# Performance work log

Hardware: AMD Instinct MI355X
Metric: run time of the kernel (lower is better)

Reference implementation:

```python
import jax, jax.numpy as jnp
import numpy as np

NUM_CLASSES = 10
SOFT_CENTER_RADIUS = 3.0
TOPK = 13
IOU_WEIGHT = 3.0
EPS = 1e-07
INF = 100000000.0


def setup_inputs() -> dict:
    key = jax.random.key(0)
    ks = jax.random.split(key, 8)
    B, N, G, C = 8, 16384, 64, NUM_CLASSES
    # priors: [N,4] = (cx, cy, stride_x, stride_y)
    centers = jax.random.uniform(ks[0], (N, 2), minval=0.0, maxval=640.0)
    strides = jnp.full((N, 2), 16.0, dtype=jnp.float32)
    priors = jnp.concatenate([centers, strides], axis=-1)
    # 2D gt boxes (x1,y1,x2,y2) inside a 640px image
    xy = jax.random.uniform(ks[1], (B, G, 2), minval=0.0, maxval=520.0)
    wh = jax.random.uniform(ks[2], (B, G, 2), minval=20.0, maxval=120.0)
    gt_bboxes = jnp.concatenate([xy, xy + wh], axis=-1)
    gt_center = xy + 0.5 * wh
    # 3D boxes: only columns [0,2] (x,z) are used by the dist iou branch
    gt_bboxes_3d = jax.random.normal(ks[3], (B, G, 7)) * 2.0
    pred_bboxes = jax.random.normal(ks[4], (B, N, 7)) * 2.0
    pred_scores = jax.random.normal(ks[5], (B, N, C))
    gt_labels = jax.random.randint(ks[6], (B, G, 1), 0, C, dtype=jnp.int32)
    pad_bbox_flag = jnp.ones((B, G, 1), dtype=jnp.float32)
    return dict(pred_bboxes=pred_bboxes, pred_scores=pred_scores, priors=priors,
                gt_labels=gt_labels, gt_bboxes=gt_bboxes, gt_center=gt_center,
                gt_bboxes_3d=gt_bboxes_3d, pad_bbox_flag=pad_bbox_flag)


def reference(pred_bboxes, pred_scores, priors, gt_labels, gt_bboxes, gt_center,
              gt_bboxes_3d, pad_bbox_flag):
    B, N, _ = pred_bboxes.shape
    G = gt_bboxes.shape[1]

    pc = priors[:, :2]                                   # [N,2]
    # find_inside_points: prior center strictly inside 2D gt box -> [B,N,G]
    cx, cy = pc[None, :, None, 0], pc[None, :, None, 1]
    inside = ((cx > gt_bboxes[:, None, :, 0]) & (cy > gt_bboxes[:, None, :, 1]) &
              (cx < gt_bboxes[:, None, :, 2]) & (cy < gt_bboxes[:, None, :, 3]))
    is_in_gts = inside.astype(jnp.float32) * pad_bbox_flag[:, None, :, 0]  # [B,N,G]
    mask = is_in_gts > 0

    # soft center prior
    strides = priors[None, :, None, 2:]                  # [1,N,1,2]
    diff = (pc[None, :, None, :] - gt_center[:, None, :, :]) / strides
    distance = jnp.linalg.norm(diff, axis=-1) * is_in_gts
    soft_center_prior = 10.0 ** (distance - SOFT_CENTER_RADIUS)

    # dist-type pairwise iou on (x,z) plane
    xz = jnp.array([0, 2])
    pxz = pred_bboxes[:, :, xz]                          # [B,N,2]
    gxz = gt_bboxes_3d[:, :, xz]                         # [B,G,2]
    d = jnp.linalg.norm(pxz[:, :, None, :] - gxz[:, None, :, :], axis=-1)
    pairwise_ious = jnp.clip(1.0 - d / 4.0, 0.0, 1.0)    # [B,N,G]

    iou_cost = -jnp.log(pairwise_ious + EPS) * IOU_WEIGHT

    labels = gt_labels[..., 0]                           # [B,G]
    idx = jnp.broadcast_to(labels[:, None, :], (B, N, G))
    pscores = jnp.take_along_axis(pred_scores, idx, axis=2)  # [B,N,G] logits
    scale = pairwise_ious - jax.nn.sigmoid(pscores)
    # stable BCE-with-logits(pscores, target=pairwise_ious)
    bce = jnp.maximum(pscores, 0.0) - pscores * pairwise_ious + jnp.log1p(jnp.exp(-jnp.abs(pscores)))
    cls_cost = bce * scale ** 2

    cost = jnp.where(mask, cls_cost + iou_cost + soft_center_prior, INF)

    # ---- dynamic k matching ----
    k = min(TOPK, N)
    topk_ious = jax.lax.top_k(jnp.swapaxes(pairwise_ious, 1, 2), k)[0]  # [B,G,k]
    dynamic_ks = jnp.clip(topk_ious.sum(-1).astype(jnp.int32), 1, None)  # [B,G]
    sorted_cost = jnp.sort(cost, axis=1)
    cost_k = jnp.take_along_axis(sorted_cost, dynamic_ks[:, None, :], axis=1)
    cost_k_1 = jnp.take_along_axis(sorted_cost, (dynamic_ks - 1)[:, None, :], axis=1)
    thr = 0.5 * (cost_k + cost_k_1) * is_in_gts          # [B,N,G]
    matching = cost <= thr                               # bool [B,N,G]
    masked_cost = jnp.where(matching, cost, INF)
    multi = matching.sum(-1) > 1                         # prior matched to >1 gt
    argmin_gt = jnp.argmin(masked_cost, axis=2)
    onehot = jax.nn.one_hot(argmin_gt, G, dtype=jnp.bool_)
    matching = jnp.where(multi[..., None], onehot, matching)

    # ---- assemble outputs (dense, jit-friendly version of nonzero indices) ----
    max_index = jnp.argmin(cost, axis=2)                 # [B,N]
    assign_metrics = jnp.take_along_axis(pairwise_ious, max_index[..., None], axis=2)[..., 0]
    matched = matching.any(-1)                           # [B,N]
    gt_idx = jnp.argmax(matching, axis=-1)               # [B,N]
    matched_iou = jnp.take_along_axis(pairwise_ious, gt_idx[..., None], axis=2)[..., 0]
    assign_metrics = jnp.where(matched, matched_iou, assign_metrics)

    assigned_labels = jnp.take_along_axis(labels, max_index, axis=1)  # [B,N]
    assigned_labels = jnp.where(assign_metrics < 1e-07, NUM_CLASSES, assigned_labels)
    assigned_labels = jnp.where(matched, jnp.take_along_axis(labels, gt_idx, axis=1), assigned_labels)

    assigned_labels_weights = jnp.ones((B, N), dtype=jnp.float32)
    return assigned_labels, assigned_labels_weights, assign_metrics, matching
```

## Files before the change

### kernel.cpp

```cpp
#include <hip/hip_runtime.h>
#include <hip/hip_bf16.h>
#include <stdint.h>

#define NCLS 10
#define B_ 8
#define N_ 16384
#define G_ 64
#define INF_ 1.0e8f

typedef unsigned long long u64;
typedef unsigned int u32;

__device__ __forceinline__ u32 ordf(float f) {
    u32 b = __float_as_uint(f);
    return (b & 0x80000000u) ? ~b : (b | 0x80000000u);
}
__device__ __forceinline__ float unordf(u32 u) {
    u32 b = (u & 0x80000000u) ? (u ^ 0x80000000u) : ~u;
    return __uint_as_float(b);
}

__device__ __forceinline__ float iou_pair(float px, float pz, float g3x, float g3z) {
#pragma clang fp contract(off)
    float ddx = px - g3x;
    float ddz = pz - g3z;
    float d = sqrtf(ddx * ddx + ddz * ddz);
    float iou = 1.0f - d / 4.0f;
    return fminf(fmaxf(iou, 0.0f), 1.0f);
}

__device__ __forceinline__ float cost_pair(float cx, float cy, float sx, float sy,
                                           float ps, float gcx, float gcy,
                                           float pad, float iou) {
#pragma clang fp contract(off)
    float dx = (cx - gcx) / sx;
    float dy = (cy - gcy) / sy;
    float dist = sqrtf(dx * dx + dy * dy) * pad;
    float soft = exp10f(dist - 3.0f);
    float iou_cost = -logf(iou + 1e-7f) * 3.0f;
    float e = expf(-fabsf(ps));
    float sig = (ps >= 0.0f) ? (1.0f / (1.0f + e)) : (e / (1.0f + e));
    float scale = iou - sig;
    float bce = fmaxf(ps, 0.0f) - ps * iou + log1pf(e);
    float cls = bce * (scale * scale);
    return cls + iou_cost + soft;
}

__device__ __forceinline__ u32 wave_max_u32(u32 k) {
#pragma unroll
    for (int off = 32; off >= 1; off >>= 1) {
        u32 o = __shfl_xor(k, off, 64);
        k = (o > k) ? o : k;
    }
    return k;
}
__device__ __forceinline__ u32 wave_min_u32(u32 k) {
#pragma unroll
    for (int off = 32; off >= 1; off >>= 1) {
        u32 o = __shfl_xor(k, off, 64);
        k = (o < k) ? o : k;
    }
    return k;
}

__global__ __launch_bounds__(256) void kP(
    const float* __restrict__ priors,
    const float* __restrict__ gt_bboxes,
    const float* __restrict__ pad_flag,
    const float* __restrict__ pred_bboxes,
    u64* __restrict__ mask64,
    u64* __restrict__ bitmapT,
    float2* __restrict__ pxz)
{
    int tid = threadIdx.x;
    int lane = tid & 63;
    if (blockIdx.x < 512) {
        int q = blockIdx.x;
        int b = q >> 6;
        int n = ((q & 63) << 8) | tid;
        u32 wword = ((q & 63) << 2) | (u32)(tid >> 6);
        float4 pr = ((const float4*)priors)[n];
        float cx = pr.x, cy = pr.y;
        u64 m = 0;
        for (int g = 0; g < G_; ++g) {
            int gi = b * G_ + g;
            float4 gbb = ((const float4*)gt_bboxes)[gi];
            float padv = pad_flag[gi];
            bool isin = (cx > gbb.x) && (cy > gbb.y) && (cx < gbb.z) && (cy < gbb.w)
                        && (padv > 0.0f);
            m |= ((u64)isin) << g;
            u64 bal = __ballot(isin);
            if (lane == 0) bitmapT[(((size_t)gi) << 8) | wword] = bal;
        }
        mask64[(size_t)b * N_ + n] = m;
    } else {
        int base = (int)(blockIdx.x - 512) * 2048 + tid;
#pragma unroll
        for (int i = 0; i < 8; ++i) {
            int idx = base + i * 256;
            float2 v;
            v.x = pred_bboxes[(size_t)idx * 7 + 0];
            v.y = pred_bboxes[(size_t)idx * 7 + 2];
            pxz[idx] = v;
        }
    }
}

#define CSWAPD(a, b) { float _h = fmaxf(a, b), _l = fminf(a, b); a = _h; b = _l; }

__global__ __launch_bounds__(256) void k1b(
    const float2* __restrict__ pxz,
    const float* __restrict__ gt_b3d,
    float* __restrict__ iou13)
{
    int wid = ((int)blockIdx.x << 2) | (threadIdx.x >> 6);
    int lane = threadIdx.x & 63;
    int b = wid >> 11;
    int g = (wid >> 5) & 63;
    int chunk = wid & 31;
    int gi = b * G_ + g;
    float g3x = gt_b3d[gi * 7 + 0];
    float g3z = gt_b3d[gi * 7 + 2];
    const float2* pp = pxz + (size_t)b * N_ + (size_t)(chunk * 512 + lane);

    float2 e0 = pp[0],   e1 = pp[64],  e2 = pp[128], e3 = pp[192];
    float2 e4 = pp[256], e5 = pp[320], e6 = pp[384], e7 = pp[448];
    float s0 = iou_pair(e0.x, e0.y, g3x, g3z);
    float s1 = iou_pair(e1.x, e1.y, g3x, g3z);
    float s2 = iou_pair(e2.x, e2.y, g3x, g3z);
    float s3 = iou_pair(e3.x, e3.y, g3x, g3z);
    float s4 = iou_pair(e4.x, e4.y, g3x, g3z);
    float s5 = iou_pair(e5.x, e5.y, g3x, g3z);
    float s6 = iou_pair(e6.x, e6.y, g3x, g3z);
    float s7 = iou_pair(e7.x, e7.y, g3x, g3z);

    CSWAPD(s0, s1) CSWAPD(s2, s3) CSWAPD(s4, s5) CSWAPD(s6, s7)
    CSWAPD(s0, s2) CSWAPD(s1, s3) CSWAPD(s4, s6) CSWAPD(s5, s7)
    CSWAPD(s1, s2) CSWAPD(s5, s6)
    CSWAPD(s0, s4) CSWAPD(s1, s5) CSWAPD(s2, s6) CSWAPD(s3, s7)
    CSWAPD(s2, s4) CSWAPD(s3, s5)
    CSWAPD(s1, s2) CSWAPD(s3, s4) CSWAPD(s5, s6)

    float keepv = 0.0f;
    for (int r = 0; r < 13; ++r) {
        u32 mykey = ordf(s0);
        u32 m = wave_max_u32(mykey);
        if (lane == r) keepv = unordf(m);
        int winner = __ffsll(__ballot(mykey == m)) - 1;
        bool win = (lane == winner);
        s0 = win ? s1 : s0;
        s1 = win ? s2 : s1;
        s2 = win ? s3 : s2;
        s3 = win ? s4 : s3;
        s4 = win ? s5 : s4;
        s5 = win ? s6 : s5;
        s6 = win ? s7 : s6;
        s7 = win ? -3.0e38f : s7;
    }
    if (lane < 13) iou13[(size_t)gi * 416 + chunk * 13 + lane] = keepv;
}

__global__ __launch_bounds__(256) void k1c(
    const float* __restrict__ iou13,
    const u64*   __restrict__ bitmapT,
    const float* __restrict__ priors,
    const float2* __restrict__ pxz,
    const float* __restrict__ pred_scores,
    const int*   __restrict__ gt_labels,
    const float* __restrict__ gt_center,
    const float* __restrict__ gt_b3d,
    const float* __restrict__ pad_flag,
    float* __restrict__ thr_half)
{
    __shared__ float s_i[4 * 13];
    __shared__ float s_c[4 * 14];
    int gi = blockIdx.x;
    int b = gi >> 6;
    int lane = threadIdx.x & 63;
    int w = threadIdx.x >> 6;

    const float* base = iou13 + (size_t)gi * 416 + w * 104;
    float v0 = base[lane];
    float v1 = (lane < 40) ? base[64 + lane] : -3.0e38f;
    if (v1 > v0) { float t = v0; v0 = v1; v1 = t; }
    {
        float keepv = 0.0f;
        for (int r = 0; r < 13; ++r) {
            u32 mykey = ordf(v0);
            u32 m = wave_max_u32(mykey);
            if (lane == r) keepv = unordf(m);
            int winner = __ffsll(__ballot(mykey == m)) - 1;
            if (lane == winner) { v0 = v1; v1 = -3.0e38f; }
        }
        if (lane < 13) s_i[w * 13 + lane] = keepv;
    }

    float gcx = gt_center[gi * 2 + 0], gcy = gt_center[gi * 2 + 1];
    float g3x = gt_b3d[gi * 7 + 0],   g3z = gt_b3d[gi * 7 + 2];
    float padv = pad_flag[gi];
    int lab = gt_labels[gi];
    const float2* pp = pxz + (size_t)b * N_;
    const float* sc = pred_scores + (size_t)b * N_ * 10;

    float l[14];
#pragma unroll
    for (int j = 0; j < 14; ++j) l[j] = INF_;
    {
        u32 word = (u32)(w * 64 + lane);
        u64 wv = bitmapT[(((size_t)gi) << 8) | word];
        u32 nb = word << 6;
        while (wv) {
            int bit = __ffsll(wv) - 1;
            wv &= wv - 1;
            int n = (int)(nb | (u32)bit);
            float4 pr = ((const float4*)priors)[n];
            float2 v = pp[n];
            float ps = sc[n * 10 + lab];
            float iou = iou_pair(v.x, v.y, g3x, g3z);
            float cst = cost_pair(pr.x, pr.y, pr.z, pr.w, ps, gcx, gcy, padv, iou);
            if (cst < l[13]) {
                float vv = cst;
#pragma unroll
                for (int jj = 0; jj < 14; ++jj) {
                    float o = l[jj]; bool lt = vv < o;
                    float mn = lt ? vv : o; vv = lt ? o : vv; l[jj] = mn;
                }
            }
        }
    }
    {
        float keepc = 0.0f;
        for (int r = 0; r < 14; ++r) {
            u32 mykey = ordf(l[0]);
            u32 m = wave_min_u32(mykey);
            if (lane == r) keepc = unordf(m);
            int winner = __ffsll(__ballot(mykey == m)) - 1;
            if (lane == winner) {
#pragma unroll
                for (int j = 0; j < 13; ++j) l[j] = l[j + 1];
                l[13] = 3.0e38f;
            }
        }
        if (lane < 14) s_c[w * 14 + lane] = keepc;
    }
    __syncthreads();

    if (w == 0) {
        float vi = (lane < 52) ? s_i[lane] : -3.0e38f;
        float sum13 = 0.0f;
        for (int r = 0; r < 13; ++r) {
            u32 mykey = ordf(vi);
            u32 m = wave_max_u32(mykey);
            sum13 += unordf(m);
            int winner = __ffsll(__ballot(mykey == m)) - 1;
            if (lane == winner) vi = -3.0e38f;
        }
        int ks = (int)sum13;
        if (ks < 1) ks = 1;

        float vc = (lane < 56) ? s_c[lane] : 3.0e38f;
        float ck = INF_, ckm1 = INF_;
        for (int r = 0; r < 14; ++r) {
            u32 mykey = ordf(vc);
            u32 m = wave_min_u32(mykey);
            float vm = unordf(m);
            if (r == ks - 1) ckm1 = vm;
            if (r == ks)     ck = vm;
            int winner = __ffsll(__ballot(mykey == m)) - 1;
            if (lane == winner) vc = 3.0e38f;
        }
        if (lane == 0) thr_half[gi] = 0.5f * (ck + ckm1);
    }
}

__global__ __launch_bounds__(256) void k2(
    const float* __restrict__ priors,
    const float2* __restrict__ pxz,
    const float* __restrict__ pred_scores,
    const int*   __restrict__ gt_labels,
    const float* __restrict__ gt_center,
    const float* __restrict__ gt_b3d,
    const float* __restrict__ pad_flag,
    const float* __restrict__ thr_half,
    const u64*   __restrict__ mask64,
    float* __restrict__ out)
{
    __shared__ float s_gcx[G_], s_gcy[G_], s_g3x[G_], s_g3z[G_];
    __shared__ float s_pad[G_], s_thr[G_];
    __shared__ int   s_lab[G_];
    __shared__ u64   s_words[256];

    int b = blockIdx.x >> 6;
    int n0b = (blockIdx.x & 63) << 8;
    int n = n0b | threadIdx.x;
    size_t t = (size_t)b * N_ + n;

    if (threadIdx.x < G_) {
        int gi = b * G_ + threadIdx.x;
        s_gcx[threadIdx.x] = gt_center[gi * 2 + 0];
        s_gcy[threadIdx.x] = gt_center[gi * 2 + 1];
        s_g3x[threadIdx.x] = gt_b3d[gi * 7 + 0];
        s_g3z[threadIdx.x] = gt_b3d[gi * 7 + 2];
        s_pad[threadIdx.x] = pad_flag[gi];
        s_thr[threadIdx.x] = thr_half[gi];
        s_lab[threadIdx.x] = gt_labels[gi];
    }
    __syncthreads();

    const float* sc = pred_scores + (size_t)b * N_ * 10;
    float4 pr = ((const float4*)priors)[n];
    float2 v2p = pxz[(size_t)b * N_ + n];
    float px = v2p.x;
    float pz = v2p.y;

    float iouC = iou_pair(px, pz, s_g3x[0], s_g3z[0]);
    float costC = INF_;
    int   labC = s_lab[0];

    float iouM = 0.0f, costM = 3.0e38f;
    int   labM = 0, argM = 0;
    u64 mmatch = 0;

    u64 m = mask64[t];
    while (m) {
        int g = __ffsll(m) - 1;
        m &= m - 1;
        float gcx = s_gcx[g], gcy = s_gcy[g];
        float g3x = s_g3x[g], g3z = s_g3z[g];
        float padg = s_pad[g];
        int   labg = s_lab[g];
        float th = s_thr[g];
        float ps = sc[n * 10 + labg];
        float iou = iou_pair(px, pz, g3x, g3z);
        float c = cost_pair(pr.x, pr.y, pr.z, pr.w, ps, gcx, gcy, padg, iou);
        if (c < costC) { costC = c; iouC = iou; labC = labg; }
        if (c <= th * padg) {
            mmatch |= 1ull << g;
            if (c < costM) { costM = c; iouM = iou; labM = labg; argM = g; }
        }
    }
    int cm = __popcll(mmatch);
    bool matched = cm > 0;
    u64 outm = (cm > 1) ? (1ull << argM) : mmatch;
    float metric = matched ? iouM : iouC;
    float olab = matched ? (float)labM
                         : ((iouC < 1e-7f) ? (float)NCLS : (float)labC);

    float* out_lab = out;
    float* out_w   = out + (size_t)B_ * N_;
    float* out_met = out + (size_t)2 * B_ * N_;
    float* out_mat = out + (size_t)3 * B_ * N_;
    out_lab[t] = olab;
    out_w[t]   = 1.0f;
    out_met[t] = metric;
    s_words[threadIdx.x] = outm;
    __syncthreads();

    int q  = threadIdx.x & 3;
    int r0 = threadIdx.x >> 2;
    size_t rowbase = (size_t)b * N_ + n0b;
#pragma unroll
    for (int it = 0; it < 4; ++it) {
        int row = r0 + (it << 6);
        u64 wv = s_words[row];
        u32 bits = (u32)(wv >> (q * 16)) & 0xffffu;
        float* dst = out_mat + (rowbase + row) * 64 + q * 16;
#pragma unroll
        for (int jj = 0; jj < 4; ++jj) {
            float4 f;
            f.x = (bits >> (jj * 4 + 0)) & 1u ? 1.0f : 0.0f;
            f.y = (bits >> (jj * 4 + 1)) & 1u ? 1.0f : 0.0f;
            f.z = (bits >> (jj * 4 + 2)) & 1u ? 1.0f : 0.0f;
            f.w = (bits >> (jj * 4 + 3)) & 1u ? 1.0f : 0.0f;
            ((float4*)dst)[jj] = f;
        }
    }
}

extern "C" void kernel_launch(void* const* d_in, const int* in_sizes, int n_in,
                              void* d_out, int out_size, void* d_ws, size_t ws_size,
                              hipStream_t stream)
{
    const float* pred_bboxes = (const float*)d_in[0];
    const float* pred_scores = (const float*)d_in[1];
    const float* priors      = (const float*)d_in[2];
    const int*   gt_labels   = (const int*)d_in[3];
    const float* gt_bboxes   = (const float*)d_in[4];
    const float* gt_center   = (const float*)d_in[5];
    const float* gt_b3d      = (const float*)d_in[6];
    const float* pad_flag    = (const float*)d_in[7];
    float* out = (float*)d_out;

    char* ws = (char*)d_ws;
    u64* mask64   = (u64*)ws;
    u64* bitmapT  = (u64*)(ws + 1048576);
    float2* pxz   = (float2*)(ws + 2097152);
    float* iou13  = (float*)(ws + 3145728);
    float* thr_half = (float*)(ws + 3145728 + 851968);

    kP<<<576, 256, 0, stream>>>(priors, gt_bboxes, pad_flag, pred_bboxes,
                                mask64, bitmapT, pxz);
    k1b<<<4096, 256, 0, stream>>>(pxz, gt_b3d, iou13);
    k1c<<<512, 256, 0, stream>>>(iou13, bitmapT, priors, pxz,
                                 pred_scores, gt_labels, gt_center, gt_b3d,
                                 pad_flag, thr_half);
    k2<<<512, 256, 0, stream>>>(priors, pxz, pred_scores, gt_labels,
                                gt_center, gt_b3d, pad_flag,
                                thr_half, mask64, out);
}
```

Measured before the change: 82.65 us.

## Fuse four assigner kernels into one cooperative kernel with grid syncs

Replaces the four separate launches (mask/bitmap build, per-chunk IoU top-13, per-gt threshold, per-prior assignment) with a single cooperative kernel of 512 blocks that uses grid.sync between phases. The per-gt IoU top-13 now runs inside one block per gt, with the partial top-13 lists kept in shared memory instead of a global iou13 buffer. This removes launch gaps and a global round trip, but drops from 4096 blocks to 512 for the IoU phase, so each block does 8x more serial work, and it adds grid-wide barrier cost.

```diff
diff --git a/kernel.cpp b/kernel.cpp
--- a/kernel.cpp
+++ b/kernel.cpp
@@ -1,6 +1,9 @@
 #include <hip/hip_runtime.h>
+#include <hip/hip_cooperative_groups.h>
 #include <hip/hip_bf16.h>
 #include <stdint.h>
+
+namespace cg = cooperative_groups;
 
 #define NCLS 10
 #define B_ 8
@@ -63,23 +66,43 @@
     return k;
 }
 
-__global__ __launch_bounds__(256) void kP(
+#define CSWAPD(a, b) { float _h = fmaxf(a, b), _l = fminf(a, b); a = _h; b = _l; }
+
+__global__ __launch_bounds__(256) void kfused(
+    const float* __restrict__ pred_bboxes,
+    const float* __restrict__ pred_scores,
     const float* __restrict__ priors,
+    const int*   __restrict__ gt_labels,
     const float* __restrict__ gt_bboxes,
+    const float* __restrict__ gt_center,
+    const float* __restrict__ gt_b3d,
     const float* __restrict__ pad_flag,
-    const float* __restrict__ pred_bboxes,
     u64* __restrict__ mask64,
     u64* __restrict__ bitmapT,
-    float2* __restrict__ pxz)
+    float2* __restrict__ pxz,
+    float* __restrict__ thr_half,
+    float* __restrict__ out)
 {
+    cg::grid_group grid = cg::this_grid();
+
+    __shared__ float s_part[416];
+    __shared__ float s_i[52], s_c[56];
+    __shared__ float s_gcx[G_], s_gcy[G_], s_g3x[G_], s_g3z[G_];
+    __shared__ float s_pad[G_], s_thr[G_];
+    __shared__ int   s_lab[G_];
+    __shared__ u64   s_words[256];
+
     int tid = threadIdx.x;
     int lane = tid & 63;
-    if (blockIdx.x < 512) {
-        int q = blockIdx.x;
-        int b = q >> 6;
-        int n = ((q & 63) << 8) | tid;
-        u32 wword = ((q & 63) << 2) | (u32)(tid >> 6);
-        float4 pr = ((const float4*)priors)[n];
+    int w = tid >> 6;
+    int q = blockIdx.x;
+    int b = q >> 6;
+    int nsl = ((q & 63) << 8) | tid;
+    size_t t = (size_t)b * N_ + nsl;
+
+    {
+        u32 wword = ((q & 63) << 2) | (u32)w;
+        float4 pr = ((const float4*)priors)[nsl];
         float cx = pr.x, cy = pr.y;
         u64 m = 0;
         for (int g = 0; g < G_; ++g) {
@@ -92,98 +115,62 @@
             u64 bal = __ballot(isin);
             if (lane == 0) bitmapT[(((size_t)gi) << 8) | wword] = bal;
         }
-        mask64[(size_t)b * N_ + n] = m;
-    } else {
-        int base = (int)(blockIdx.x - 512) * 2048 + tid;
-#pragma unroll
-        for (int i = 0; i < 8; ++i) {
-            int idx = base + i * 256;
-            float2 v;
-            v.x = pred_bboxes[(size_t)idx * 7 + 0];
-            v.y = pred_bboxes[(size_t)idx * 7 + 2];
-            pxz[idx] = v;
-        }
-    }
-}
-
-#define CSWAPD(a, b) { float _h = fmaxf(a, b), _l = fminf(a, b); a = _h; b = _l; }
-
-__global__ __launch_bounds__(256) void k1b(
-    const float2* __restrict__ pxz,
-    const float* __restrict__ gt_b3d,
-    float* __restrict__ iou13)
-{
-    int wid = ((int)blockIdx.x << 2) | (threadIdx.x >> 6);
-    int lane = threadIdx.x & 63;
-    int b = wid >> 11;
-    int g = (wid >> 5) & 63;
-    int chunk = wid & 31;
-    int gi = b * G_ + g;
+        mask64[t] = m;
+        float2 v;
+        v.x = pred_bboxes[t * 7 + 0];
+        v.y = pred_bboxes[t * 7 + 2];
+        pxz[t] = v;
+    }
+    grid.sync();
+
+    int gi = q;
     float g3x = gt_b3d[gi * 7 + 0];
     float g3z = gt_b3d[gi * 7 + 2];
-    const float2* pp = pxz + (size_t)b * N_ + (size_t)(chunk * 512 + lane);
-
-    float2 e0 = pp[0],   e1 = pp[64],  e2 = pp[128], e3 = pp[192];
-    float2 e4 = pp[256], e5 = pp[320], e6 = pp[384], e7 = pp[448];
-    float s0 = iou_pair(e0.x, e0.y, g3x, g3z);
-    float s1 = iou_pair(e1.x, e1.y, g3x, g3z);
-    float s2 = iou_pair(e2.x, e2.y, g3x, g3z);
-    float s3 = iou_pair(e3.x, e3.y, g3x, g3z);
-    float s4 = iou_pair(e4.x, e4.y, g3x, g3z);
-    float s5 = iou_pair(e5.x, e5.y, g3x, g3z);
-    float s6 = iou_pair(e6.x, e6.y, g3x, g3z);
-    float s7 = iou_pair(e7.x, e7.y, g3x, g3z);
-
-    CSWAPD(s0, s1) CSWAPD(s2, s3) CSWAPD(s4, s5) CSWAPD(s6, s7)
-    CSWAPD(s0, s2) CSWAPD(s1, s3) CSWAPD(s4, s6) CSWAPD(s5, s7)
-    CSWAPD(s1, s2) CSWAPD(s5, s6)
-    CSWAPD(s0, s4) CSWAPD(s1, s5) CSWAPD(s2, s6) CSWAPD(s3, s7)
-    CSWAPD(s2, s4) CSWAPD(s3, s5)
-    CSWAPD(s1, s2) CSWAPD(s3, s4) CSWAPD(s5, s6)
-
-    float keepv = 0.0f;
-    for (int r = 0; r < 13; ++r) {
-        u32 mykey = ordf(s0);
-        u32 m = wave_max_u32(mykey);
-        if (lane == r) keepv = unordf(m);
-        int winner = __ffsll(__ballot(mykey == m)) - 1;
-        bool win = (lane == winner);
-        s0 = win ? s1 : s0;
-        s1 = win ? s2 : s1;
-        s2 = win ? s3 : s2;
-        s3 = win ? s4 : s3;
-        s4 = win ? s5 : s4;
-        s5 = win ? s6 : s5;
-        s6 = win ? s7 : s6;
-        s7 = win ? -3.0e38f : s7;
-    }
-    if (lane < 13) iou13[(size_t)gi * 416 + chunk * 13 + lane] = keepv;
-}
-
-__global__ __launch_bounds__(256) void k1c(
-    const float* __restrict__ iou13,
-    const u64*   __restrict__ bitmapT,
-    const float* __restrict__ priors,
-    const float2* __restrict__ pxz,
-    const float* __restrict__ pred_scores,
-    const int*   __restrict__ gt_labels,
-    const float* __restrict__ gt_center,
-    const float* __restrict__ gt_b3d,
-    const float* __restrict__ pad_flag,
-    float* __restrict__ thr_half)
-{
-    __shared__ float s_i[4 * 13];
-    __shared__ float s_c[4 * 14];
-    int gi = blockIdx.x;
-    int b = gi >> 6;
-    int lane = threadIdx.x & 63;
-    int w = threadIdx.x >> 6;
-
-    const float* base = iou13 + (size_t)gi * 416 + w * 104;
-    float v0 = base[lane];
-    float v1 = (lane < 40) ? base[64 + lane] : -3.0e38f;
-    if (v1 > v0) { float t = v0; v0 = v1; v1 = t; }
-    {
+    const float2* pp = pxz + (size_t)b * N_;
+    for (int c8 = 0; c8 < 8; ++c8) {
+        int chunk = w * 8 + c8;
+        const float2* p0 = pp + (size_t)(chunk * 512 + lane);
+        float2 e0 = p0[0],   e1 = p0[64],  e2 = p0[128], e3 = p0[192];
+        float2 e4 = p0[256], e5 = p0[320], e6 = p0[384], e7 = p0[448];
+        float s0 = iou_pair(e0.x, e0.y, g3x, g3z);
+        float s1 = iou_pair(e1.x, e1.y, g3x, g3z);
+        float s2 = iou_pair(e2.x, e2.y, g3x, g3z);
+        float s3 = iou_pair(e3.x, e3.y, g3x, g3z);
+        float s4 = iou_pair(e4.x, e4.y, g3x, g3z);
+        float s5 = iou_pair(e5.x, e5.y, g3x, g3z);
+        float s6 = iou_pair(e6.x, e6.y, g3x, g3z);
+        float s7 = iou_pair(e7.x, e7.y, g3x, g3z);
+        CSWAPD(s0, s1) CSWAPD(s2, s3) CSWAPD(s4, s5) CSWAPD(s6, s7)
+        CSWAPD(s0, s2) CSWAPD(s1, s3) CSWAPD(s4, s6) CSWAPD(s5, s7)
+        CSWAPD(s1, s2) CSWAPD(s5, s6)
+        CSWAPD(s0, s4) CSWAPD(s1, s5) CSWAPD(s2, s6) CSWAPD(s3, s7)
+        CSWAPD(s2, s4) CSWAPD(s3, s5)
+        CSWAPD(s1, s2) CSWAPD(s3, s4) CSWAPD(s5, s6)
+        float keepv = 0.0f;
+        for (int r = 0; r < 13; ++r) {
+            u32 mykey = ordf(s0);
+            u32 m = wave_max_u32(mykey);
+            if (lane == r) keepv = unordf(m);
+            int winner = __ffsll(__ballot(mykey == m)) - 1;
+            bool win = (lane == winner);
+            s0 = win ? s1 : s0;
+            s1 = win ? s2 : s1;
+            s2 = win ? s3 : s2;
+            s3 = win ? s4 : s3;
+            s4 = win ? s5 : s4;
+            s5 = win ? s6 : s5;
+            s6 = win ? s7 : s6;
+            s7 = win ? -3.0e38f : s7;
+        }
+        if (lane < 13) s_part[chunk * 13 + lane] = keepv;
+    }
+    __syncthreads();
+
+    {
+        const float* basep = s_part + w * 104;
+        float v0 = basep[lane];
+        float v1 = (lane < 40) ? basep[64 + lane] : -3.0e38f;
+        if (v1 > v0) { float tt = v0; v0 = v1; v1 = tt; }
         float keepv = 0.0f;
         for (int r = 0; r < 13; ++r) {
             u32 mykey = ordf(v0);
@@ -194,21 +181,17 @@
         }
         if (lane < 13) s_i[w * 13 + lane] = keepv;
     }
-
-    float gcx = gt_center[gi * 2 + 0], gcy = gt_center[gi * 2 + 1];
-    float g3x = gt_b3d[gi * 7 + 0],   g3z = gt_b3d[gi * 7 + 2];
-    float padv = pad_flag[gi];
-    int lab = gt_labels[gi];
-    const float2* pp = pxz + (size_t)b * N_;
-    const float* sc = pred_scores + (size_t)b * N_ * 10;
-
-    float l[14];
-#pragma unroll
-    for (int j = 0; j < 14; ++j) l[j] = INF_;
-    {
-        u32 word = (u32)(w * 64 + lane);
-        u64 wv = bitmapT[(((size_t)gi) << 8) | word];
-        u32 nb = word << 6;
+    {
+        float gcx = gt_center[gi * 2 + 0], gcy = gt_center[gi * 2 + 1];
+        float padv = pad_flag[gi];
+        int lab = gt_labels[gi];
+        const float* sc = pred_scores + (size_t)b * N_ * 10;
+
+        float l[14];
+#pragma unroll
+        for (int j = 0; j < 14; ++j) l[j] = INF_;
+        u64 wv = bitmapT[(((size_t)gi) << 8) | (u32)tid];
+        u32 nb = (u32)tid << 6;
         while (wv) {
             int bit = __ffsll(wv) - 1;
             wv &= wv - 1;
@@ -227,8 +210,6 @@
                 }
             }
         }
-    }
-    {
         float keepc = 0.0f;
         for (int r = 0; r < 14; ++r) {
             u32 mykey = ordf(l[0]);
@@ -271,108 +252,91 @@
         }
         if (lane == 0) thr_half[gi] = 0.5f * (ck + ckm1);
     }
-}
-
-__global__ __launch_bounds__(256) void k2(
-    const float* __restrict__ priors,
-    const float2* __restrict__ pxz,
-    const float* __restrict__ pred_scores,
-    const int*   __restrict__ gt_labels,
-    const float* __restrict__ gt_center,
-    const float* __restrict__ gt_b3d,
-    const float* __restrict__ pad_flag,
-    const float* __restrict__ thr_half,
-    const u64*   __restrict__ mask64,
-    float* __restrict__ out)
-{
-    __shared__ float s_gcx[G_], s_gcy[G_], s_g3x[G_], s_g3z[G_];
-    __shared__ float s_pad[G_], s_thr[G_];
-    __shared__ int   s_lab[G_];
-    __shared__ u64   s_words[256];
-
-    int b = blockIdx.x >> 6;
-    int n0b = (blockIdx.x & 63) << 8;
-    int n = n0b | threadIdx.x;
-    size_t t = (size_t)b * N_ + n;
-
-    if (threadIdx.x < G_) {
-        int gi = b * G_ + threadIdx.x;
-        s_gcx[threadIdx.x] = gt_center[gi * 2 + 0];
-        s_gcy[threadIdx.x] = gt_center[gi * 2 + 1];
-        s_g3x[threadIdx.x] = gt_b3d[gi * 7 + 0];
-        s_g3z[threadIdx.x] = gt_b3d[gi * 7 + 2];
-        s_pad[threadIdx.x] = pad_flag[gi];
-        s_thr[threadIdx.x] = thr_half[gi];
-        s_lab[threadIdx.x] = gt_labels[gi];
+    grid.sync();
+
+    if (tid < G_) {
+        int gg = b * G_ + tid;
+        s_gcx[tid] = gt_center[gg * 2 + 0];
+        s_gcy[tid] = gt_center[gg * 2 + 1];
+        s_g3x[tid] = gt_b3d[gg * 7 + 0];
+        s_g3z[tid] = gt_b3d[gg * 7 + 2];
+        s_pad[tid] = pad_flag[gg];
+        s_thr[tid] = thr_half[gg];
+        s_lab[tid] = gt_labels[gg];
     }
     __syncthreads();
 
-    const float* sc = pred_scores + (size_t)b * N_ * 10;
-    float4 pr = ((const float4*)priors)[n];
-    float2 v2p = pxz[(size_t)b * N_ + n];
-    float px = v2p.x;
-    float pz = v2p.y;
-
-    float iouC = iou_pair(px, pz, s_g3x[0], s_g3z[0]);
-    float costC = INF_;
-    int   labC = s_lab[0];
-
-    float iouM = 0.0f, costM = 3.0e38f;
-    int   labM = 0, argM = 0;
-    u64 mmatch = 0;
-
-    u64 m = mask64[t];
-    while (m) {
-        int g = __ffsll(m) - 1;
-        m &= m - 1;
-        float gcx = s_gcx[g], gcy = s_gcy[g];
-        float g3x = s_g3x[g], g3z = s_g3z[g];
-        float padg = s_pad[g];
-        int   labg = s_lab[g];
-        float th = s_thr[g];
-        float ps = sc[n * 10 + labg];
-        float iou = iou_pair(px, pz, g3x, g3z);
-        float c = cost_pair(pr.x, pr.y, pr.z, pr.w, ps, gcx, gcy, padg, iou);
-        if (c < costC) { costC = c; iouC = iou; labC = labg; }
-        if (c <= th * padg) {
-            mmatch |= 1ull << g;
-            if (c < costM) { costM = c; iouM = iou; labM = labg; argM = g; }
-        }
-    }
-    int cm = __popcll(mmatch);
-    bool matched = cm > 0;
-    u64 outm = (cm > 1) ? (1ull << argM) : mmatch;
-    float metric = matched ? iouM : iouC;
-    float olab = matched ? (float)labM
-                         : ((iouC < 1e-7f) ? (float)NCLS : (float)labC);
-
-    float* out_lab = out;
-    float* out_w   = out + (size_t)B_ * N_;
-    float* out_met = out + (size_t)2 * B_ * N_;
-    float* out_mat = out + (size_t)3 * B_ * N_;
-    out_lab[t] = olab;
-    out_w[t]   = 1.0f;
-    out_met[t] = metric;
-    s_words[threadIdx.x] = outm;
+    {
+        const float* sc = pred_scores + (size_t)b * N_ * 10;
+        float4 pr = ((const float4*)priors)[nsl];
+        float2 v2p = pxz[t];
+        float px = v2p.x;
+        float pz = v2p.y;
+
+        float iouC = iou_pair(px, pz, s_g3x[0], s_g3z[0]);
+        float costC = INF_;
+        int   labC = s_lab[0];
+
+        float iouM = 0.0f, costM = 3.0e38f;
+        int   labM = 0, argM = 0;
+        u64 mmatch = 0;
+
+        u64 m = mask64[t];
+        while (m) {
+            int g = __ffsll(m) - 1;
+            m &= m - 1;
+            float gcx = s_gcx[g], gcy = s_gcy[g];
+            float g3xx = s_g3x[g], g3zz = s_g3z[g];
+            float padg = s_pad[g];
+            int   labg = s_lab[g];
+            float th = s_thr[g];
+            float ps = sc[nsl * 10 + labg];
+            float iou = iou_pair(px, pz, g3xx, g3zz);
+            float c = cost_pair(pr.x, pr.y, pr.z, pr.w, ps, gcx, gcy, padg, iou);
+            if (c < costC) { costC = c; iouC = iou; labC = labg; }
+            if (c <= th * padg) {
+                mmatch |= 1ull << g;
+                if (c < costM) { costM = c; iouM = iou; labM = labg; argM = g; }
+            }
+        }
+        int cm = __popcll(mmatch);
+        bool matched = cm > 0;
+        u64 outm = (cm > 1) ? (1ull << argM) : mmatch;
+        float metric = matched ? iouM : iouC;
+        float olab = matched ? (float)labM
+                             : ((iouC < 1e-7f) ? (float)NCLS : (float)labC);
+
+        float* out_lab = out;
+        float* out_w   = out + (size_t)B_ * N_;
+        float* out_met = out + (size_t)2 * B_ * N_;
+        float* out_mat = out + (size_t)3 * B_ * N_;
+        out_lab[t] = olab;
+        out_w[t]   = 1.0f;
+        out_met[t] = metric;
+        s_words[tid] = outm;
+    }
     __syncthreads();
 
-    int q  = threadIdx.x & 3;
-    int r0 = threadIdx.x >> 2;
-    size_t rowbase = (size_t)b * N_ + n0b;
-#pragma unroll
-    for (int it = 0; it < 4; ++it) {
-        int row = r0 + (it << 6);
-        u64 wv = s_words[row];
-        u32 bits = (u32)(wv >> (q * 16)) & 0xffffu;
-        float* dst = out_mat + (rowbase + row) * 64 + q * 16;
-#pragma unroll
-        for (int jj = 0; jj < 4; ++jj) {
-            float4 f;
-            f.x = (bits >> (jj * 4 + 0)) & 1u ? 1.0f : 0.0f;
-            f.y = (bits >> (jj * 4 + 1)) & 1u ? 1.0f : 0.0f;
-            f.z = (bits >> (jj * 4 + 2)) & 1u ? 1.0f : 0.0f;
-            f.w = (bits >> (jj * 4 + 3)) & 1u ? 1.0f : 0.0f;
-            ((float4*)dst)[jj] = f;
+    {
+        float* out_mat = out + (size_t)3 * B_ * N_;
+        int qq = tid & 3;
+        int r0 = tid >> 2;
+        size_t rowbase = (size_t)b * N_ + ((q & 63) << 8);
+#pragma unroll
+        for (int it = 0; it < 4; ++it) {
+            int row = r0 + (it << 6);
+            u64 wv = s_words[row];
+            u32 bits = (u32)(wv >> (qq * 16)) & 0xffffu;
+            float* dst = out_mat + (rowbase + row) * 64 + qq * 16;
+#pragma unroll
+            for (int jj = 0; jj < 4; ++jj) {
+                float4 f;
+                f.x = (bits >> (jj * 4 + 0)) & 1u ? 1.0f : 0.0f;
+                f.y = (bits >> (jj * 4 + 1)) & 1u ? 1.0f : 0.0f;
+                f.z = (bits >> (jj * 4 + 2)) & 1u ? 1.0f : 0.0f;
+                f.w = (bits >> (jj * 4 + 3)) & 1u ? 1.0f : 0.0f;
+                ((float4*)dst)[jj] = f;
+            }
         }
     }
 }
@@ -395,16 +359,15 @@
     u64* mask64   = (u64*)ws;
     u64* bitmapT  = (u64*)(ws + 1048576);
     float2* pxz   = (float2*)(ws + 2097152);
-    float* iou13  = (float*)(ws + 3145728);
-    float* thr_half = (float*)(ws + 3145728 + 851968);
-
-    kP<<<576, 256, 0, stream>>>(priors, gt_bboxes, pad_flag, pred_bboxes,
-                                mask64, bitmapT, pxz);
-    k1b<<<4096, 256, 0, stream>>>(pxz, gt_b3d, iou13);
-    k1c<<<512, 256, 0, stream>>>(iou13, bitmapT, priors, pxz,
-                                 pred_scores, gt_labels, gt_center, gt_b3d,
-                                 pad_flag, thr_half);
-    k2<<<512, 256, 0, stream>>>(priors, pxz, pred_scores, gt_labels,
-                                gt_center, gt_b3d, pad_flag,
-                                thr_half, mask64, out);
-}
+    float* thr_half = (float*)(ws + 3145728);
+
+    void* args[] = {
+        (void*)&pred_bboxes, (void*)&pred_scores, (void*)&priors,
+        (void*)&gt_labels, (void*)&gt_bboxes, (void*)&gt_center,
+        (void*)&gt_b3d, (void*)&pad_flag,
+        (void*)&mask64, (void*)&bitmapT, (void*)&pxz, (void*)&thr_half,
+        (void*)&out
+    };
+    hipLaunchCooperativeKernel((const void*)kfused, dim3(512), dim3(256),
+                               args, 0, stream);
+}
```

Result: slower. 192.4 us (+132.8%).

## Recompute inside-gt masks in consumers instead of precomputing bitmaps

Applied to the files above, without the earlier changes.

Drops the separate prior-in-box pass that wrote the per-prior mask and the transposed per-gt bitmap. The per-gt top-14 cost kernel now scans all 16384 priors itself and tests box containment inline, using a branchless fixed-register insertion network. The final assignment kernel recomputes its 64-bit mask per prior before the shared-memory barrier. This removes one kernel's output traffic and its dependency, but k1c now does a full scan of all priors per gt instead of visiting only the set bits.

```diff
diff --git a/kernel.cpp b/kernel.cpp
--- a/kernel.cpp
+++ b/kernel.cpp
@@ -63,50 +63,23 @@
     return k;
 }
 
-__global__ __launch_bounds__(256) void kP(
-    const float* __restrict__ priors,
-    const float* __restrict__ gt_bboxes,
-    const float* __restrict__ pad_flag,
+#define INSA(a, v) { float _l = fminf(a, v), _h = fmaxf(a, v); a = _l; v = _h; }
+#define CSWAPD(a, b) { float _h = fmaxf(a, b), _l = fminf(a, b); a = _h; b = _l; }
+
+__global__ __launch_bounds__(256) void kPack(
     const float* __restrict__ pred_bboxes,
-    u64* __restrict__ mask64,
-    u64* __restrict__ bitmapT,
     float2* __restrict__ pxz)
 {
-    int tid = threadIdx.x;
-    int lane = tid & 63;
-    if (blockIdx.x < 512) {
-        int q = blockIdx.x;
-        int b = q >> 6;
-        int n = ((q & 63) << 8) | tid;
-        u32 wword = ((q & 63) << 2) | (u32)(tid >> 6);
-        float4 pr = ((const float4*)priors)[n];
-        float cx = pr.x, cy = pr.y;
-        u64 m = 0;
-        for (int g = 0; g < G_; ++g) {
-            int gi = b * G_ + g;
-            float4 gbb = ((const float4*)gt_bboxes)[gi];
-            float padv = pad_flag[gi];
-            bool isin = (cx > gbb.x) && (cy > gbb.y) && (cx < gbb.z) && (cy < gbb.w)
-                        && (padv > 0.0f);
-            m |= ((u64)isin) << g;
-            u64 bal = __ballot(isin);
-            if (lane == 0) bitmapT[(((size_t)gi) << 8) | wword] = bal;
-        }
-        mask64[(size_t)b * N_ + n] = m;
-    } else {
-        int base = (int)(blockIdx.x - 512) * 2048 + tid;
-#pragma unroll
-        for (int i = 0; i < 8; ++i) {
-            int idx = base + i * 256;
-            float2 v;
-            v.x = pred_bboxes[(size_t)idx * 7 + 0];
-            v.y = pred_bboxes[(size_t)idx * 7 + 2];
-            pxz[idx] = v;
-        }
-    }
-}
-
-#define CSWAPD(a, b) { float _h = fmaxf(a, b), _l = fminf(a, b); a = _h; b = _l; }
+    int base = (int)blockIdx.x * 2048 + threadIdx.x;
+#pragma unroll
+    for (int i = 0; i < 8; ++i) {
+        int idx = base + i * 256;
+        float2 v;
+        v.x = pred_bboxes[(size_t)idx * 7 + 0];
+        v.y = pred_bboxes[(size_t)idx * 7 + 2];
+        pxz[idx] = v;
+    }
+}
 
 __global__ __launch_bounds__(256) void k1b(
     const float2* __restrict__ pxz,
@@ -162,11 +135,11 @@
 
 __global__ __launch_bounds__(256) void k1c(
     const float* __restrict__ iou13,
-    const u64*   __restrict__ bitmapT,
     const float* __restrict__ priors,
     const float2* __restrict__ pxz,
     const float* __restrict__ pred_scores,
     const int*   __restrict__ gt_labels,
+    const float* __restrict__ gt_bboxes,
     const float* __restrict__ gt_center,
     const float* __restrict__ gt_b3d,
     const float* __restrict__ pad_flag,
@@ -176,8 +149,9 @@
     __shared__ float s_c[4 * 14];
     int gi = blockIdx.x;
     int b = gi >> 6;
-    int lane = threadIdx.x & 63;
-    int w = threadIdx.x >> 6;
+    int tid = threadIdx.x;
+    int lane = tid & 63;
+    int w = tid >> 6;
 
     const float* base = iou13 + (size_t)gi * 416 + w * 104;
     float v0 = base[lane];
@@ -195,6 +169,8 @@
         if (lane < 13) s_i[w * 13 + lane] = keepv;
     }
 
+    float gx1 = gt_bboxes[gi * 4 + 0], gy1 = gt_bboxes[gi * 4 + 1];
+    float gx2 = gt_bboxes[gi * 4 + 2], gy2 = gt_bboxes[gi * 4 + 3];
     float gcx = gt_center[gi * 2 + 0], gcy = gt_center[gi * 2 + 1];
     float g3x = gt_b3d[gi * 7 + 0],   g3z = gt_b3d[gi * 7 + 2];
     float padv = pad_flag[gi];
@@ -202,44 +178,37 @@
     const float2* pp = pxz + (size_t)b * N_;
     const float* sc = pred_scores + (size_t)b * N_ * 10;
 
-    float l[14];
-#pragma unroll
-    for (int j = 0; j < 14; ++j) l[j] = INF_;
-    {
-        u32 word = (u32)(w * 64 + lane);
-        u64 wv = bitmapT[(((size_t)gi) << 8) | word];
-        u32 nb = word << 6;
-        while (wv) {
-            int bit = __ffsll(wv) - 1;
-            wv &= wv - 1;
-            int n = (int)(nb | (u32)bit);
-            float4 pr = ((const float4*)priors)[n];
+    float c0 = INF_, c1 = INF_, c2 = INF_, c3 = INF_, c4 = INF_,
+          c5 = INF_, c6 = INF_, c7 = INF_, c8 = INF_, c9 = INF_,
+          c10 = INF_, c11 = INF_, c12 = INF_, c13 = INF_;
+    for (int it = 0; it < 64; ++it) {
+        int n = (it << 8) | tid;
+        float4 pr = ((const float4*)priors)[n];
+        bool isin = (pr.x > gx1) && (pr.y > gy1) && (pr.x < gx2) && (pr.y < gy2)
+                    && (padv > 0.0f);
+        if (isin) {
             float2 v = pp[n];
             float ps = sc[n * 10 + lab];
             float iou = iou_pair(v.x, v.y, g3x, g3z);
-            float cst = cost_pair(pr.x, pr.y, pr.z, pr.w, ps, gcx, gcy, padv, iou);
-            if (cst < l[13]) {
-                float vv = cst;
-#pragma unroll
-                for (int jj = 0; jj < 14; ++jj) {
-                    float o = l[jj]; bool lt = vv < o;
-                    float mn = lt ? vv : o; vv = lt ? o : vv; l[jj] = mn;
-                }
-            }
+            float u = cost_pair(pr.x, pr.y, pr.z, pr.w, ps, gcx, gcy, padv, iou);
+            INSA(c0, u) INSA(c1, u) INSA(c2, u) INSA(c3, u) INSA(c4, u)
+            INSA(c5, u) INSA(c6, u) INSA(c7, u) INSA(c8, u) INSA(c9, u)
+            INSA(c10, u) INSA(c11, u) INSA(c12, u) INSA(c13, u)
         }
     }
     {
         float keepc = 0.0f;
         for (int r = 0; r < 14; ++r) {
-            u32 mykey = ordf(l[0]);
+            u32 mykey = ordf(c0);
             u32 m = wave_min_u32(mykey);
             if (lane == r) keepc = unordf(m);
             int winner = __ffsll(__ballot(mykey == m)) - 1;
-            if (lane == winner) {
-#pragma unroll
-                for (int j = 0; j < 13; ++j) l[j] = l[j + 1];
-                l[13] = 3.0e38f;
-            }
+            bool win = (lane == winner);
+            c0 = win ? c1 : c0;   c1 = win ? c2 : c1;   c2 = win ? c3 : c2;
+            c3 = win ? c4 : c3;   c4 = win ? c5 : c4;   c5 = win ? c6 : c5;
+            c6 = win ? c7 : c6;   c7 = win ? c8 : c7;   c8 = win ? c9 : c8;
+            c9 = win ? c10 : c9;  c10 = win ? c11 : c10; c11 = win ? c12 : c11;
+            c12 = win ? c13 : c12; c13 = win ? 3.0e38f : c13;
         }
         if (lane < 14) s_c[w * 14 + lane] = keepc;
     }
@@ -278,11 +247,11 @@
     const float2* __restrict__ pxz,
     const float* __restrict__ pred_scores,
     const int*   __restrict__ gt_labels,
+    const float* __restrict__ gt_bboxes,
     const float* __restrict__ gt_center,
     const float* __restrict__ gt_b3d,
     const float* __restrict__ pad_flag,
     const float* __restrict__ thr_half,
-    const u64*   __restrict__ mask64,
     float* __restrict__ out)
 {
     __shared__ float s_gcx[G_], s_gcy[G_], s_g3x[G_], s_g3z[G_];
@@ -305,13 +274,24 @@
         s_thr[threadIdx.x] = thr_half[gi];
         s_lab[threadIdx.x] = gt_labels[gi];
     }
-    __syncthreads();
 
     const float* sc = pred_scores + (size_t)b * N_ * 10;
     float4 pr = ((const float4*)priors)[n];
-    float2 v2p = pxz[(size_t)b * N_ + n];
+    float2 v2p = pxz[t];
     float px = v2p.x;
     float pz = v2p.y;
+
+    u64 m = 0;
+#pragma unroll 8
+    for (int g = 0; g < G_; ++g) {
+        int gi = b * G_ + g;
+        float4 gbb = ((const float4*)gt_bboxes)[gi];
+        float padv = pad_flag[gi];
+        bool isin = (pr.x > gbb.x) && (pr.y > gbb.y) && (pr.x < gbb.z)
+                    && (pr.y < gbb.w) && (padv > 0.0f);
+        m |= ((u64)isin) << g;
+    }
+    __syncthreads();
 
     float iouC = iou_pair(px, pz, s_g3x[0], s_g3z[0]);
     float costC = INF_;
@@ -321,7 +301,6 @@
     int   labM = 0, argM = 0;
     u64 mmatch = 0;
 
-    u64 m = mask64[t];
     while (m) {
         int g = __ffsll(m) - 1;
         m &= m - 1;
@@ -392,19 +371,16 @@
     float* out = (float*)d_out;
 
     char* ws = (char*)d_ws;
-    u64* mask64   = (u64*)ws;
-    u64* bitmapT  = (u64*)(ws + 1048576);
-    float2* pxz   = (float2*)(ws + 2097152);
-    float* iou13  = (float*)(ws + 3145728);
-    float* thr_half = (float*)(ws + 3145728 + 851968);
-
-    kP<<<576, 256, 0, stream>>>(priors, gt_bboxes, pad_flag, pred_bboxes,
-                                mask64, bitmapT, pxz);
+    float2* pxz   = (float2*)ws;
+    float* iou13  = (float*)(ws + 1048576);
+    float* thr_half = (float*)(ws + 1048576 + 851968);
+
+    kPack<<<64, 256, 0, stream>>>(pred_bboxes, pxz);
     k1b<<<4096, 256, 0, stream>>>(pxz, gt_b3d, iou13);
-    k1c<<<512, 256, 0, stream>>>(iou13, bitmapT, priors, pxz,
-                                 pred_scores, gt_labels, gt_center, gt_b3d,
-                                 pad_flag, thr_half);
+    k1c<<<512, 256, 0, stream>>>(iou13, priors, pxz, pred_scores, gt_labels,
+                                 gt_bboxes, gt_center, gt_b3d, pad_flag,
+                                 thr_half);
     k2<<<512, 256, 0, stream>>>(priors, pxz, pred_scores, gt_labels,
-                                gt_center, gt_b3d, pad_flag,
-                                thr_half, mask64, out);
-}
+                                gt_bboxes, gt_center, gt_b3d, pad_flag,
+                                thr_half, out);
+}
```

Result: slower. 136.7 us (+65.4%).
